# Optimization experiments

Measured on AMD Instinct MI355X. Metric: run time of the kernel, lower is better.

The kernel has to match this reference:

```python
import jax, jax.numpy as jnp
import numpy as np

# Model constants (match init_kwargs)
DIM = 256
H = 8
HD = DIM // H          # 32
WIN = 5                # spatial window_size
QS = 4                 # quant_size
CQS = 2 * QS           # color_quant_size = 8
CWIN = 2               # color_windowsize
W = 64                 # voxels per window (equal-size windows for the reference)
L_XYZ = WIN * QS       # 20 -> table length 40
L_RGB = CWIN * CQS     # 16 -> table length 32


def setup_inputs() -> dict:
    key = jax.random.key(0)
    ks = jax.random.split(key, 12)
    N = 8192
    feats = jax.random.normal(ks[0], (N, DIM), dtype=jnp.float32)
    xyz = jax.random.uniform(ks[1], (N, 3), dtype=jnp.float32) * WIN    # [0, window_size)
    rgb = jax.random.uniform(ks[2], (N, 3), dtype=jnp.float32) * CWIN   # [0, color_windowsize)
    n_coords = jnp.concatenate([xyz, rgb], axis=1)
    std = 0.02
    xyz_shape = (3, 2 * L_XYZ, H, HD)
    rgb_shape = (3, 2 * L_RGB, H, HD)
    return {
        "feats": feats,
        "n_coords": n_coords,
        "qkv_w": jax.random.normal(ks[3], (3 * DIM, DIM), dtype=jnp.float32) * std,
        "qkv_b": jnp.zeros((3 * DIM,), dtype=jnp.float32),
        "q_xyz_t": jax.random.normal(ks[4], xyz_shape, dtype=jnp.float32) * std,
        "k_xyz_t": jax.random.normal(ks[5], xyz_shape, dtype=jnp.float32) * std,
        "v_xyz_t": jax.random.normal(ks[6], xyz_shape, dtype=jnp.float32) * std,
        "q_rgb_t": jax.random.normal(ks[7], rgb_shape, dtype=jnp.float32) * std,
        "k_rgb_t": jax.random.normal(ks[8], rgb_shape, dtype=jnp.float32) * std,
        "v_rgb_t": jax.random.normal(ks[9], rgb_shape, dtype=jnp.float32) * std,
        "proj_w": jax.random.normal(ks[10], (DIM, DIM), dtype=jnp.float32) * std,
        "proj_b": jnp.zeros((DIM,), dtype=jnp.float32),
    }


def _attn_bias(q, k, idx, q_table, k_table):
    """Relative-signal bias added to QK logits.
    q,k: [nw, W, H, hd]; idx: [nw, W, W, 3] int; tables: [3, T, H, hd].
    bias[n,h,i,j] = sum_c q[n,i,h]. q_table[c, idx[n,i,j,c], h] + k[n,j,h]. k_table[c, idx, h]
    Returns (bias [nw,H,W,W], one_hot [nw,W,W,3,T]) so the one-hot is reused for the value bias.
    """
    T = q_table.shape[1]
    oh = jax.nn.one_hot(idx, T, dtype=q.dtype)                # [nw,W,W,3,T]
    dq = jnp.einsum('nihd,cthd->nicht', q, q_table)           # per-voxel dot vs all table rows
    dk = jnp.einsum('njhd,cthd->njcht', k, k_table)
    bias_q = jnp.einsum('nicht,nijct->nhij', dq, oh)
    bias_k = jnp.einsum('njcht,nijct->nhij', dk, oh)
    return bias_q + bias_k, oh


def _value_bias(attn, oh, v_table):
    """out[n,i,h,:] += sum_j attn[n,h,i,j] * sum_c v_table[c, idx[n,i,j,c], h, :]"""
    at = jnp.einsum('nhij,nijct->nhict', attn, oh)            # scatter attn mass onto table rows
    return jnp.einsum('nhict,cthd->nihd', at, v_table)


def reference(feats, n_coords, qkv_w, qkv_b, q_xyz_t, k_xyz_t, v_xyz_t,
              q_rgb_t, k_rgb_t, v_rgb_t, proj_w, proj_b):
    N = feats.shape[0]
    nw = N // W
    scale = HD ** (-0.5)

    # QKV projection, split into per-window heads
    qkv = (feats @ qkv_w.T + qkv_b).reshape(nw, W, 3, H, HD)
    q = qkv[:, :, 0] * scale
    k = qkv[:, :, 1]
    v = qkv[:, :, 2]

    # Quantized relative-signal indices (coordinate deltas, offset to [0, 2L))
    scaled = jnp.concatenate(
        [n_coords[:, 0:3] * QS, n_coords[:, 3:6] * CQS], axis=1)   # [N, 6]
    cw = scaled.reshape(nw, W, 6)
    delta = jnp.floor(cw[:, :, None, :] - cw[:, None, :, :]).astype(jnp.int32)
    offs = jnp.array([L_XYZ] * 3 + [L_RGB] * 3, dtype=jnp.int32)
    hi = jnp.array([2 * L_XYZ - 1] * 3 + [2 * L_RGB - 1] * 3, dtype=jnp.int32)
    idx = jnp.clip(delta + offs, 0, hi)                        # [nw, W, W, 6]
    idx_xyz, idx_rgb = idx[..., :3], idx[..., 3:]

    bias_x, oh_x = _attn_bias(q, k, idx_xyz, q_xyz_t, k_xyz_t)
    bias_r, oh_r = _attn_bias(q, k, idx_rgb, q_rgb_t, k_rgb_t)

    logits = jnp.einsum('nihd,njhd->nhij', q, k) + bias_x + bias_r
    attn = jax.nn.softmax(logits, axis=-1)

    out = (jnp.einsum('nhij,njhd->nihd', attn, v)
           + _value_bias(attn, oh_x, v_xyz_t)
           + _value_bias(attn, oh_r, v_rgb_t))
    out = out.reshape(N, DIM)
    return out @ proj_w.T + proj_b
```

## Files before the change

kernel.cpp:

```cpp
#include <hip/hip_runtime.h>


typedef __attribute__((ext_vector_type(8))) short short8;
typedef __attribute__((ext_vector_type(4))) float f32x4;

__device__ __forceinline__ unsigned short f2bf(float f) {
    union { float f; unsigned int u; } v; v.f = f;
    unsigned int r = v.u + 0x7FFFu + ((v.u >> 16) & 1u);
    return (unsigned short)(r >> 16);
}

#define LFENCE() asm volatile("s_waitcnt lgkmcnt(0)" ::: "memory")

__global__ __launch_bounds__(256) void k_cast(
    const float* __restrict__ feats, const float* __restrict__ qkvw,
    const float* __restrict__ pw,
    ushort* __restrict__ fb, ushort* __restrict__ qwb, ushort* __restrict__ pwb)
{
    int t = blockIdx.x * 256 + threadIdx.x;
    const float* src; ushort* dst; int off;
    if (t < 262144)            { src = feats; dst = fb;  off = t; }
    else if (t < 286720)       { src = qkvw;  dst = qwb; off = t - 262144; }
    else                       { src = pw;    dst = pwb; off = t - 286720; }
    const float* s = src + (size_t)off * 8;
    float4 v0 = *(const float4*)s, v1 = *(const float4*)(s + 4);
    union { ushort u[8]; uint4 v; } pk;
    pk.u[0] = f2bf(v0.x); pk.u[1] = f2bf(v0.y); pk.u[2] = f2bf(v0.z); pk.u[3] = f2bf(v0.w);
    pk.u[4] = f2bf(v1.x); pk.u[5] = f2bf(v1.y); pk.u[6] = f2bf(v1.z); pk.u[7] = f2bf(v1.w);
    *(uint4*)(dst + (size_t)off * 8) = pk.v;
}

__global__ __launch_bounds__(256) void k_qkv(
    const ushort* __restrict__ A, const ushort* __restrict__ B,
    const float* __restrict__ bias,
    ushort* __restrict__ qb, ushort* __restrict__ kb, ushort* __restrict__ vb)
{
    __shared__ __align__(16) ushort a_s[64 * 72];
    __shared__ __align__(16) ushort b_s[64 * 72];
    const int tid = threadIdx.x;
    const int m0 = blockIdx.y * 64;
    const int n0 = blockIdx.x * 64;
    const int w = tid >> 6, wm = w >> 1, wn = w & 1;
    const int l4 = tid & 15, quad = (tid >> 4) & 3;
    f32x4 acc[2][2];
#pragma unroll
    for (int mt = 0; mt < 2; ++mt)
#pragma unroll
        for (int nt = 0; nt < 2; ++nt) acc[mt][nt] = (f32x4){0.f, 0.f, 0.f, 0.f};

    for (int k0 = 0; k0 < 256; k0 += 64) {
#pragma unroll
        for (int l = 0; l < 2; ++l) {
            int e = tid + l * 256;
            int row = e >> 3, kq = e & 7;
            *(uint4*)&a_s[row * 72 + kq * 8] =
                *(const uint4*)(A + (size_t)(m0 + row) * 256 + k0 + kq * 8);
            *(uint4*)&b_s[row * 72 + kq * 8] =
                *(const uint4*)(B + (size_t)(n0 + row) * 256 + k0 + kq * 8);
        }
        __syncthreads();
#pragma unroll
        for (int kh = 0; kh < 2; ++kh) {
            short8 bf0 = *(const short8*)&b_s[(wn * 32 + l4) * 72 + kh * 32 + quad * 8];
            short8 bf1 = *(const short8*)&b_s[(wn * 32 + 16 + l4) * 72 + kh * 32 + quad * 8];
#pragma unroll
            for (int mt = 0; mt < 2; ++mt) {
                short8 af = *(const short8*)&a_s[(wm * 32 + mt * 16 + l4) * 72 + kh * 32 + quad * 8];
                acc[mt][0] = __builtin_amdgcn_mfma_f32_16x16x32_bf16(af, bf0, acc[mt][0], 0, 0, 0);
                acc[mt][1] = __builtin_amdgcn_mfma_f32_16x16x32_bf16(af, bf1, acc[mt][1], 0, 0, 0);
            }
        }
        __syncthreads();
    }
#pragma unroll
    for (int nt = 0; nt < 2; ++nt) {
        int c = n0 + wn * 32 + nt * 16 + l4;
        float bv = bias[c];
        int s = c >> 8, rem = c & 255, h = rem >> 5, d = rem & 31;
        ushort* dst = (s == 0) ? qb : ((s == 1) ? kb : vb);
        float mul = (s == 0) ? 0.17677669529663687f : 1.0f;
#pragma unroll
        for (int mt = 0; mt < 2; ++mt) {
            int mbase = m0 + wm * 32 + mt * 16 + quad * 4;
#pragma unroll
            for (int reg = 0; reg < 4; ++reg) {
                int m = mbase + reg;
                int nw = m >> 6, ii = m & 63;
                dst[((size_t)((nw * 8 + h) * 64 + ii)) * 32 + d] = f2bf((acc[mt][nt][reg] + bv) * mul);
            }
        }
    }
}

#define DBS 44
#define SL3 132
#define FXS 16777216.0f
#define FXI (1.0f / 16777216.0f)

__global__ __launch_bounds__(256, 2) void k_bias(
    const ushort* __restrict__ qb, const ushort* __restrict__ kb,
    const float* __restrict__ nco,
    const float* __restrict__ kxt, const float* __restrict__ krt,
    float* __restrict__ lgt)
{
    __shared__ __align__(16) float dbuf[64 * DBS];
    __shared__ __align__(16) ushort q_s[64 * 40];
    __shared__ __align__(16) ushort k_s[64 * 40];
    __shared__ __align__(16) ushort tbl[128 * 40];
    __shared__ __align__(16) float cwf[64 * 6];

    const int tid = threadIdx.x;
    const int n = blockIdx.x >> 3;
    const int h = blockIdx.x & 7;
    const int w = tid >> 6;
    const int l4 = tid & 15;
    const int quad = (tid >> 4) & 3;

    const size_t base = (size_t)((n * 8 + h) * 64) * 32;

    {
        int row = tid >> 2, part = tid & 3;
        *(uint4*)&q_s[row * 40 + part * 8] = *(const uint4*)(qb + base + tid * 8);
        *(uint4*)&k_s[row * 40 + part * 8] = *(const uint4*)(kb + base + tid * 8);
    }
    if (tid < 64) {
        const float* cp = nco + (size_t)(n * 64 + tid) * 6;
        cwf[tid * 6 + 0] = cp[0] * 4.f; cwf[tid * 6 + 1] = cp[1] * 4.f;
        cwf[tid * 6 + 2] = cp[2] * 4.f; cwf[tid * 6 + 3] = cp[3] * 8.f;
        cwf[tid * 6 + 4] = cp[4] * 8.f; cwf[tid * 6 + 5] = cp[5] * 8.f;
    }

    auto stageTbl = [&](const float* tbg, int R, int Rpad) {
        for (int e = tid; e < R * 4; e += 256) {
            int r = e >> 2, part = e & 3;
            const float* src = tbg + (size_t)r * 256 + part * 8;
            float4 f0 = *(const float4*)src, f1 = *(const float4*)(src + 4);
            union { ushort u[8]; uint4 v; } pk;
            pk.u[0] = f2bf(f0.x); pk.u[1] = f2bf(f0.y); pk.u[2] = f2bf(f0.z); pk.u[3] = f2bf(f0.w);
            pk.u[4] = f2bf(f1.x); pk.u[5] = f2bf(f1.y); pk.u[6] = f2bf(f1.z); pk.u[7] = f2bf(f1.w);
            *(uint4*)&tbl[r * 40 + part * 8] = pk.v;
        }
        for (int e = tid; e < (Rpad - R) * 40; e += 256) tbl[R * 40 + e] = 0;
    };

    float lg[4][4];
    int ibase[4];
#pragma unroll
    for (int r = 0; r < 4; ++r) ibase[r] = (w * 16 + quad * 4 + r) * DBS;

    auto tgemmC = [&](const ushort* a_s, int c, int T) {
        short8 af = *(const short8*)&a_s[(w * 16 + l4) * 40 + quad * 8];
        const int NT = (T == 40) ? 3 : 2;
        for (int tt = 0; tt < NT; ++tt) {
            short8 bf = *(const short8*)&tbl[(c * T + tt * 16 + l4) * 40 + quad * 8];
            f32x4 a = {0.f, 0.f, 0.f, 0.f};
            a = __builtin_amdgcn_mfma_f32_16x16x32_bf16(af, bf, a, 0, 0, 0);
            int col = tt * 16 + l4;
            int rb = w * 16 + quad * 4;
            if (col < T) {
                dbuf[(rb + 0) * DBS + col] = a[0];
                dbuf[(rb + 1) * DBS + col] = a[1];
                dbuf[(rb + 2) * DBS + col] = a[2];
                dbuf[(rb + 3) * DBS + col] = a[3];
            }
        }
    };

    stageTbl(kxt + h * 32, 120, 128);
    __syncthreads();

    unsigned idxp[24];
#pragma unroll
    for (int c6 = 0; c6 < 6; ++c6) {
        const int off = (c6 < 3) ? 20 : 16, hi = (c6 < 3) ? 39 : 31;
        float co0 = cwf[(w * 16 + quad * 4 + 0) * 6 + c6];
        float co1 = cwf[(w * 16 + quad * 4 + 1) * 6 + c6];
        float co2 = cwf[(w * 16 + quad * 4 + 2) * 6 + c6];
        float co3 = cwf[(w * 16 + quad * 4 + 3) * 6 + c6];
#pragma unroll
        for (int tt = 0; tt < 4; ++tt) {
            float ci = cwf[(tt * 16 + l4) * 6 + c6];
            unsigned p = (unsigned)min(max((int)floorf(ci - co0) + off, 0), hi);
            p |= (unsigned)min(max((int)floorf(ci - co1) + off, 0), hi) << 8;
            p |= (unsigned)min(max((int)floorf(ci - co2) + off, 0), hi) << 16;
            p |= (unsigned)min(max((int)floorf(ci - co3) + off, 0), hi) << 24;
            idxp[c6 * 4 + tt] = p;
        }
    }

    auto gatherT = [&](int cc) {
#pragma unroll
        for (int tt = 0; tt < 4; ++tt) {
            unsigned p = idxp[cc * 4 + tt];
#pragma unroll
            for (int r = 0; r < 4; ++r) {
                int x = (p >> (8 * r)) & 255;
                lg[tt][r] += dbuf[ibase[r] + x];
            }
        }
    };

    {
        short8 ak = *(const short8*)&k_s[(w * 16 + l4) * 40 + quad * 8];
#pragma unroll
        for (int tt = 0; tt < 4; ++tt) {
            short8 bq = *(const short8*)&q_s[(tt * 16 + l4) * 40 + quad * 8];
            f32x4 r = {0.f, 0.f, 0.f, 0.f};
            r = __builtin_amdgcn_mfma_f32_16x16x32_bf16(ak, bq, r, 0, 0, 0);
            lg[tt][0] = r[0]; lg[tt][1] = r[1]; lg[tt][2] = r[2]; lg[tt][3] = r[3];
        }
    }

    tgemmC(k_s, 0, 40); LFENCE();
    gatherT(0); LFENCE();
    tgemmC(k_s, 1, 40); LFENCE();
    gatherT(1); LFENCE();
    tgemmC(k_s, 2, 40); LFENCE();
    gatherT(2);
    __syncthreads();
    stageTbl(krt + h * 32, 96, 96);
    __syncthreads();
    tgemmC(k_s, 0, 32); LFENCE();
    gatherT(3); LFENCE();
    tgemmC(k_s, 1, 32); LFENCE();
    gatherT(4); LFENCE();
    tgemmC(k_s, 2, 32); LFENCE();
    gatherT(5);

    {
        float* lp = lgt + (size_t)(n * 8 + h) * 4096;
#pragma unroll
        for (int tt = 0; tt < 4; ++tt)
#pragma unroll
            for (int reg = 0; reg < 4; ++reg)
                lp[(w * 16 + quad * 4 + reg) * 64 + tt * 16 + l4] = lg[tt][reg];
    }
}

__global__ __launch_bounds__(256, 2) void k_av(
    const ushort* __restrict__ qb, const ushort* __restrict__ vb,
    const float* __restrict__ nco,
    const float* __restrict__ qxt, const float* __restrict__ vxt,
    const float* __restrict__ qrt, const float* __restrict__ vrt,
    const float* __restrict__ lgt,
    ushort* __restrict__ aout)
{
    __shared__ __align__(16) float dbuf[64 * SL3];
    __shared__ __align__(16) ushort U[11264];
    __shared__ __align__(16) float cwf[64 * 6];
    ushort* q_s  = U;
    ushort* tbl  = U + 2560;
    ushort* attn_s = U;
    ushort* v_t    = U + 4608;
    ushort* vtbl   = U + 6912;

    const int tid = threadIdx.x;
    const int n = blockIdx.x >> 3;
    const int h = blockIdx.x & 7;
    const int w = tid >> 6;
    const int lane = tid & 63;
    const int l4 = tid & 15;
    const int quad = (tid >> 4) & 3;

    const size_t base = (size_t)((n * 8 + h) * 64) * 32;

    {
        int row = tid >> 2, part = tid & 3;
        *(uint4*)&q_s[row * 40 + part * 8] = *(const uint4*)(qb + base + tid * 8);
    }
    if (tid < 64) {
        const float* cp = nco + (size_t)(n * 64 + tid) * 6;
        cwf[tid * 6 + 0] = cp[0] * 4.f; cwf[tid * 6 + 1] = cp[1] * 4.f;
        cwf[tid * 6 + 2] = cp[2] * 4.f; cwf[tid * 6 + 3] = cp[3] * 8.f;
        cwf[tid * 6 + 4] = cp[4] * 8.f; cwf[tid * 6 + 5] = cp[5] * 8.f;
    }

    auto stageTbl = [&](const float* tbg, int R, int Rpad) {
        for (int e = tid; e < R * 4; e += 256) {
            int r = e >> 2, part = e & 3;
            const float* src = tbg + (size_t)r * 256 + part * 8;
            float4 f0 = *(const float4*)src, f1 = *(const float4*)(src + 4);
            union { ushort u[8]; uint4 v; } pk;
            pk.u[0] = f2bf(f0.x); pk.u[1] = f2bf(f0.y); pk.u[2] = f2bf(f0.z); pk.u[3] = f2bf(f0.w);
            pk.u[4] = f2bf(f1.x); pk.u[5] = f2bf(f1.y); pk.u[6] = f2bf(f1.z); pk.u[7] = f2bf(f1.w);
            *(uint4*)&tbl[r * 40 + part * 8] = pk.v;
        }
        for (int e = tid; e < (Rpad - R) * 40; e += 256) tbl[R * 40 + e] = 0;
    };
    auto stageVtbl = [&](const float* tbg, int R) {
        for (int e = tid; e < R * 4; e += 256) {
            int r = e >> 2, part = e & 3;
            const float* src = tbg + (size_t)r * 256 + part * 8;
            float4 f0 = *(const float4*)src, f1 = *(const float4*)(src + 4);
            int d0 = part * 8;
            vtbl[(d0 + 0) * 136 + r] = f2bf(f0.x);
            vtbl[(d0 + 1) * 136 + r] = f2bf(f0.y);
            vtbl[(d0 + 2) * 136 + r] = f2bf(f0.z);
            vtbl[(d0 + 3) * 136 + r] = f2bf(f0.w);
            vtbl[(d0 + 4) * 136 + r] = f2bf(f1.x);
            vtbl[(d0 + 5) * 136 + r] = f2bf(f1.y);
            vtbl[(d0 + 6) * 136 + r] = f2bf(f1.z);
            vtbl[(d0 + 7) * 136 + r] = f2bf(f1.w);
        }
    };
    auto stageVt = [&]() {
        int j = tid >> 2, d0 = (tid & 3) * 8;
        uint4 pk = *(const uint4*)(vb + base + tid * 8);
        const ushort* u = (const ushort*)&pk;
#pragma unroll
        for (int ii = 0; ii < 8; ++ii) v_t[(d0 + ii) * 72 + j] = u[ii];
    };

    float lg[4][4];
    {
        const float* lp = lgt + (size_t)(n * 8 + h) * 4096;
        int i0 = w * 16 + quad * 4;
#pragma unroll
        for (int tt = 0; tt < 4; ++tt) {
            f32x4 v = *(const f32x4*)(lp + (size_t)(tt * 16 + l4) * 64 + i0);
            lg[tt][0] = v[0]; lg[tt][1] = v[1]; lg[tt][2] = v[2]; lg[tt][3] = v[3];
        }
    }

    int ibase[4];
#pragma unroll
    for (int r = 0; r < 4; ++r) ibase[r] = (w * 16 + quad * 4 + r) * SL3;

    auto tgemm3 = [&](int T) {
        short8 af = *(const short8*)&q_s[(w * 16 + l4) * 40 + quad * 8];
        const int NT = (T == 40) ? 3 : 2;
        int rb = w * 16 + quad * 4;
#pragma unroll
        for (int c = 0; c < 3; ++c) {
            for (int tt = 0; tt < NT; ++tt) {
                short8 bf = *(const short8*)&tbl[(c * T + tt * 16 + l4) * 40 + quad * 8];
                f32x4 a = {0.f, 0.f, 0.f, 0.f};
                a = __builtin_amdgcn_mfma_f32_16x16x32_bf16(af, bf, a, 0, 0, 0);
                int col = tt * 16 + l4;
                if (col < T) {
                    int sc = c * DBS + col;
                    dbuf[(rb + 0) * SL3 + sc] = a[0];
                    dbuf[(rb + 1) * SL3 + sc] = a[1];
                    dbuf[(rb + 2) * SL3 + sc] = a[2];
                    dbuf[(rb + 3) * SL3 + sc] = a[3];
                }
            }
        }
    };
    auto zeroAll = [&]() {
        float4 z = {0.f, 0.f, 0.f, 0.f};
        float4* rb = (float4*)&dbuf[w * 16 * SL3];
        for (int v = lane; v < 528; v += 64) rb[v] = z;
    };

    stageTbl(qxt + h * 32, 120, 128);
    __syncthreads();

    unsigned idxp[24];
#pragma unroll
    for (int c6 = 0; c6 < 6; ++c6) {
        const int off = (c6 < 3) ? 20 : 16, hi = (c6 < 3) ? 39 : 31;
        float co0 = cwf[(w * 16 + quad * 4 + 0) * 6 + c6];
        float co1 = cwf[(w * 16 + quad * 4 + 1) * 6 + c6];
        float co2 = cwf[(w * 16 + quad * 4 + 2) * 6 + c6];
        float co3 = cwf[(w * 16 + quad * 4 + 3) * 6 + c6];
#pragma unroll
        for (int tt = 0; tt < 4; ++tt) {
            float cj = cwf[(tt * 16 + l4) * 6 + c6];
            unsigned p = (unsigned)min(max((int)floorf(co0 - cj) + off, 0), hi);
            p |= (unsigned)min(max((int)floorf(co1 - cj) + off, 0), hi) << 8;
            p |= (unsigned)min(max((int)floorf(co2 - cj) + off, 0), hi) << 16;
            p |= (unsigned)min(max((int)floorf(co3 - cj) + off, 0), hi) << 24;
            idxp[c6 * 4 + tt] = p;
        }
    }

    auto gather3 = [&](int half) {
#pragma unroll
        for (int c = 0; c < 3; ++c) {
#pragma unroll
            for (int tt = 0; tt < 4; ++tt) {
                unsigned p = idxp[(half * 3 + c) * 4 + tt];
#pragma unroll
                for (int r = 0; r < 4; ++r) {
                    int x = (p >> (8 * r)) & 255;
                    lg[tt][r] += dbuf[ibase[r] + c * DBS + x];
                }
            }
        }
    };
    auto scatter3 = [&](int half) {
        unsigned* bb = (unsigned*)dbuf;
#pragma unroll
        for (int c = 0; c < 3; ++c) {
#pragma unroll
            for (int tt = 0; tt < 4; ++tt) {
                unsigned p = idxp[(half * 3 + c) * 4 + tt];
#pragma unroll
                for (int r = 0; r < 4; ++r) {
                    int x = (p >> (8 * r)) & 255;
                    unsigned q = (unsigned)(lg[tt][r] * FXS + 0.5f);
                    atomicAdd(&bb[ibase[r] + c * DBS + x], q);
                }
            }
        }
    };

    tgemm3(40);
    __syncthreads();
    gather3(0);
    stageTbl(qrt + h * 32, 96, 96);
    __syncthreads();
    tgemm3(32);
    __syncthreads();
    gather3(1);
    stageVtbl(vxt + h * 32, 120);
    stageVt();
    __syncthreads();

#pragma unroll
    for (int reg = 0; reg < 4; ++reg) {
        float m = fmaxf(fmaxf(lg[0][reg], lg[1][reg]), fmaxf(lg[2][reg], lg[3][reg]));
        m = fmaxf(m, __shfl_xor(m, 1));
        m = fmaxf(m, __shfl_xor(m, 2));
        m = fmaxf(m, __shfl_xor(m, 4));
        m = fmaxf(m, __shfl_xor(m, 8));
        float s = 0.f;
#pragma unroll
        for (int tt = 0; tt < 4; ++tt) { lg[tt][reg] = __expf(lg[tt][reg] - m); s += lg[tt][reg]; }
        s += __shfl_xor(s, 1); s += __shfl_xor(s, 2);
        s += __shfl_xor(s, 4); s += __shfl_xor(s, 8);
        float inv = 1.f / s;
#pragma unroll
        for (int tt = 0; tt < 4; ++tt) lg[tt][reg] *= inv;
    }
#pragma unroll
    for (int tt = 0; tt < 4; ++tt)
#pragma unroll
        for (int reg = 0; reg < 4; ++reg)
            attn_s[(w * 16 + quad * 4 + reg) * 72 + tt * 16 + l4] = f2bf(lg[tt][reg]);
    zeroAll();
    __syncthreads();

    f32x4 acc0 = {0.f, 0.f, 0.f, 0.f}, acc1 = {0.f, 0.f, 0.f, 0.f};
#pragma unroll
    for (int s = 0; s < 2; ++s) {
        short8 af = *(const short8*)&attn_s[(w * 16 + l4) * 72 + s * 32 + quad * 8];
        short8 b0 = *(const short8*)&v_t[l4 * 72 + s * 32 + quad * 8];
        short8 b1 = *(const short8*)&v_t[(16 + l4) * 72 + s * 32 + quad * 8];
        acc0 = __builtin_amdgcn_mfma_f32_16x16x32_bf16(af, b0, acc0, 0, 0, 0);
        acc1 = __builtin_amdgcn_mfma_f32_16x16x32_bf16(af, b1, acc1, 0, 0, 0);
    }

    auto atgemm3 = [&](int T, int S) {
        int rowb = (w * 16 + l4) * SL3;
#pragma unroll
        for (int c = 0; c < 3; ++c) {
#pragma unroll
            for (int s = 0; s < S; ++s) {
                int koff = s * 32 + quad * 8;
                short8 af = {0, 0, 0, 0, 0, 0, 0, 0};
                int kr = 0;
                if (koff < T) {
                    const unsigned* ap = (const unsigned*)&dbuf[rowb + c * DBS + koff];
                    uint4 u0 = *(const uint4*)ap;
                    uint4 u1 = *(const uint4*)(ap + 4);
                    af[0] = (short)f2bf((float)u0.x * FXI); af[1] = (short)f2bf((float)u0.y * FXI);
                    af[2] = (short)f2bf((float)u0.z * FXI); af[3] = (short)f2bf((float)u0.w * FXI);
                    af[4] = (short)f2bf((float)u1.x * FXI); af[5] = (short)f2bf((float)u1.y * FXI);
                    af[6] = (short)f2bf((float)u1.z * FXI); af[7] = (short)f2bf((float)u1.w * FXI);
                    kr = c * T + koff;
                }
                short8 b0 = *(const short8*)&vtbl[l4 * 136 + kr];
                short8 b1 = *(const short8*)&vtbl[(16 + l4) * 136 + kr];
                acc0 = __builtin_amdgcn_mfma_f32_16x16x32_bf16(af, b0, acc0, 0, 0, 0);
                acc1 = __builtin_amdgcn_mfma_f32_16x16x32_bf16(af, b1, acc1, 0, 0, 0);
            }
        }
    };

    scatter3(0); LFENCE();
    atgemm3(40, 2);
    __syncthreads();
    zeroAll();
    stageVtbl(vrt + h * 32, 96);
    __syncthreads();
    scatter3(1); LFENCE();
    atgemm3(32, 1);

    {
        ushort* op = aout + (size_t)(n * 64 + w * 16 + quad * 4) * 256 + h * 32;
#pragma unroll
        for (int reg = 0; reg < 4; ++reg) {
            op[reg * 256 + l4] = f2bf(acc0[reg]);
            op[reg * 256 + 16 + l4] = f2bf(acc1[reg]);
        }
    }
}

__global__ __launch_bounds__(256) void k_proj(
    const ushort* __restrict__ A, const ushort* __restrict__ B,
    const float* __restrict__ bias, float* __restrict__ out)
{
    __shared__ __align__(16) ushort a_s[64 * 72];
    __shared__ __align__(16) ushort b_s[64 * 72];
    const int tid = threadIdx.x;
    const int m0 = blockIdx.y * 64;
    const int n0 = blockIdx.x * 64;
    const int w = tid >> 6, wm = w >> 1, wn = w & 1;
    const int l4 = tid & 15, quad = (tid >> 4) & 3;
    f32x4 acc[2][2];
#pragma unroll
    for (int mt = 0; mt < 2; ++mt)
#pragma unroll
        for (int nt = 0; nt < 2; ++nt) acc[mt][nt] = (f32x4){0.f, 0.f, 0.f, 0.f};

    for (int k0 = 0; k0 < 256; k0 += 64) {
#pragma unroll
        for (int l = 0; l < 2; ++l) {
            int e = tid + l * 256;
            int row = e >> 3, kq = e & 7;
            *(uint4*)&a_s[row * 72 + kq * 8] =
                *(const uint4*)(A + (size_t)(m0 + row) * 256 + k0 + kq * 8);
            *(uint4*)&b_s[row * 72 + kq * 8] =
                *(const uint4*)(B + (size_t)(n0 + row) * 256 + k0 + kq * 8);
        }
        __syncthreads();
#pragma unroll
        for (int kh = 0; kh < 2; ++kh) {
            short8 bf0 = *(const short8*)&b_s[(wn * 32 + l4) * 72 + kh * 32 + quad * 8];
            short8 bf1 = *(const short8*)&b_s[(wn * 32 + 16 + l4) * 72 + kh * 32 + quad * 8];
#pragma unroll
            for (int mt = 0; mt < 2; ++mt) {
                short8 af = *(const short8*)&a_s[(wm * 32 + mt * 16 + l4) * 72 + kh * 32 + quad * 8];
                acc[mt][0] = __builtin_amdgcn_mfma_f32_16x16x32_bf16(af, bf0, acc[mt][0], 0, 0, 0);
                acc[mt][1] = __builtin_amdgcn_mfma_f32_16x16x32_bf16(af, bf1, acc[mt][1], 0, 0, 0);
            }
        }
        __syncthreads();
    }
#pragma unroll
    for (int nt = 0; nt < 2; ++nt) {
        int c = n0 + wn * 32 + nt * 16 + l4;
        float bv = bias[c];
#pragma unroll
        for (int mt = 0; mt < 2; ++mt) {
            int mbase = m0 + wm * 32 + mt * 16 + quad * 4;
#pragma unroll
            for (int reg = 0; reg < 4; ++reg)
                out[(size_t)(mbase + reg) * 256 + c] = acc[mt][nt][reg] + bv;
        }
    }
}

extern "C" void kernel_launch(void* const* d_in, const int* in_sizes, int n_in,
                              void* d_out, int out_size, void* d_ws, size_t ws_size,
                              hipStream_t stream)
{
    const float* feats = (const float*)d_in[0];
    const float* nco   = (const float*)d_in[1];
    const float* qkvw  = (const float*)d_in[2];
    const float* qkvb  = (const float*)d_in[3];
    const float* qxt   = (const float*)d_in[4];
    const float* kxt   = (const float*)d_in[5];
    const float* vxt   = (const float*)d_in[6];
    const float* qrt   = (const float*)d_in[7];
    const float* krt   = (const float*)d_in[8];
    const float* vrt   = (const float*)d_in[9];
    const float* pw    = (const float*)d_in[10];
    const float* pb    = (const float*)d_in[11];
    float* out = (float*)d_out;

    ushort* qb  = (ushort*)d_ws;
    ushort* kb  = qb + (size_t)2097152;
    ushort* vb  = kb + (size_t)2097152;
    ushort* aob = vb + (size_t)2097152;
    float*  lgt = (float*)(aob + (size_t)2097152);
    ushort* fb  = (ushort*)(lgt + (size_t)4194304);
    ushort* qwb = fb + (size_t)2097152;
    ushort* pwb = qwb + (size_t)196608;

    k_cast<<<dim3(1152), 256, 0, stream>>>(feats, qkvw, pw, fb, qwb, pwb);
    k_qkv<<<dim3(12, 128), 256, 0, stream>>>(fb, qwb, qkvb, qb, kb, vb);
    k_bias<<<dim3(1024), 256, 0, stream>>>(qb, kb, nco, kxt, krt, lgt);
    k_av<<<dim3(1024), 256, 0, stream>>>(qb, vb, nco, qxt, vxt, qrt, vrt, lgt, aob);
    k_proj<<<dim3(4, 128), 256, 0, stream>>>(aob, pwb, pb, out);
}
```

Baseline: 148.4 us.

## Fuse key-bias logits kernel into attention kernel, dropping logits round-trip

Merges the separate key-side bias kernel into the attention/value kernel, so QK logits and both key and query table biases are computed in registers within one block. This removes a 16 MB fp32 logits write and read through global memory and one kernel launch. In exchange the fused kernel does more serial work per block, with extra table staging and syncthreads, and it must fit K in the same shared buffer, which may lengthen each block.

```diff
diff --git a/kernel.cpp b/kernel.cpp
--- a/kernel.cpp
+++ b/kernel.cpp
@@ -97,159 +97,19 @@
 #define FXS 16777216.0f
 #define FXI (1.0f / 16777216.0f)
 
-__global__ __launch_bounds__(256, 2) void k_bias(
-    const ushort* __restrict__ qb, const ushort* __restrict__ kb,
+__global__ __launch_bounds__(256, 2) void k_attn(
+    const ushort* __restrict__ qb, const ushort* __restrict__ kb, const ushort* __restrict__ vb,
     const float* __restrict__ nco,
-    const float* __restrict__ kxt, const float* __restrict__ krt,
-    float* __restrict__ lgt)
-{
-    __shared__ __align__(16) float dbuf[64 * DBS];
-    __shared__ __align__(16) ushort q_s[64 * 40];
-    __shared__ __align__(16) ushort k_s[64 * 40];
-    __shared__ __align__(16) ushort tbl[128 * 40];
-    __shared__ __align__(16) float cwf[64 * 6];
-
-    const int tid = threadIdx.x;
-    const int n = blockIdx.x >> 3;
-    const int h = blockIdx.x & 7;
-    const int w = tid >> 6;
-    const int l4 = tid & 15;
-    const int quad = (tid >> 4) & 3;
-
-    const size_t base = (size_t)((n * 8 + h) * 64) * 32;
-
-    {
-        int row = tid >> 2, part = tid & 3;
-        *(uint4*)&q_s[row * 40 + part * 8] = *(const uint4*)(qb + base + tid * 8);
-        *(uint4*)&k_s[row * 40 + part * 8] = *(const uint4*)(kb + base + tid * 8);
-    }
-    if (tid < 64) {
-        const float* cp = nco + (size_t)(n * 64 + tid) * 6;
-        cwf[tid * 6 + 0] = cp[0] * 4.f; cwf[tid * 6 + 1] = cp[1] * 4.f;
-        cwf[tid * 6 + 2] = cp[2] * 4.f; cwf[tid * 6 + 3] = cp[3] * 8.f;
-        cwf[tid * 6 + 4] = cp[4] * 8.f; cwf[tid * 6 + 5] = cp[5] * 8.f;
-    }
-
-    auto stageTbl = [&](const float* tbg, int R, int Rpad) {
-        for (int e = tid; e < R * 4; e += 256) {
-            int r = e >> 2, part = e & 3;
-            const float* src = tbg + (size_t)r * 256 + part * 8;
-            float4 f0 = *(const float4*)src, f1 = *(const float4*)(src + 4);
-            union { ushort u[8]; uint4 v; } pk;
-            pk.u[0] = f2bf(f0.x); pk.u[1] = f2bf(f0.y); pk.u[2] = f2bf(f0.z); pk.u[3] = f2bf(f0.w);
-            pk.u[4] = f2bf(f1.x); pk.u[5] = f2bf(f1.y); pk.u[6] = f2bf(f1.z); pk.u[7] = f2bf(f1.w);
-            *(uint4*)&tbl[r * 40 + part * 8] = pk.v;
-        }
-        for (int e = tid; e < (Rpad - R) * 40; e += 256) tbl[R * 40 + e] = 0;
-    };
-
-    float lg[4][4];
-    int ibase[4];
-#pragma unroll
-    for (int r = 0; r < 4; ++r) ibase[r] = (w * 16 + quad * 4 + r) * DBS;
-
-    auto tgemmC = [&](const ushort* a_s, int c, int T) {
-        short8 af = *(const short8*)&a_s[(w * 16 + l4) * 40 + quad * 8];
-        const int NT = (T == 40) ? 3 : 2;
-        for (int tt = 0; tt < NT; ++tt) {
-            short8 bf = *(const short8*)&tbl[(c * T + tt * 16 + l4) * 40 + quad * 8];
-            f32x4 a = {0.f, 0.f, 0.f, 0.f};
-            a = __builtin_amdgcn_mfma_f32_16x16x32_bf16(af, bf, a, 0, 0, 0);
-            int col = tt * 16 + l4;
-            int rb = w * 16 + quad * 4;
-            if (col < T) {
-                dbuf[(rb + 0) * DBS + col] = a[0];
-                dbuf[(rb + 1) * DBS + col] = a[1];
-                dbuf[(rb + 2) * DBS + col] = a[2];
-                dbuf[(rb + 3) * DBS + col] = a[3];
-            }
-        }
-    };
-
-    stageTbl(kxt + h * 32, 120, 128);
-    __syncthreads();
-
-    unsigned idxp[24];
-#pragma unroll
-    for (int c6 = 0; c6 < 6; ++c6) {
-        const int off = (c6 < 3) ? 20 : 16, hi = (c6 < 3) ? 39 : 31;
-        float co0 = cwf[(w * 16 + quad * 4 + 0) * 6 + c6];
-        float co1 = cwf[(w * 16 + quad * 4 + 1) * 6 + c6];
-        float co2 = cwf[(w * 16 + quad * 4 + 2) * 6 + c6];
-        float co3 = cwf[(w * 16 + quad * 4 + 3) * 6 + c6];
-#pragma unroll
-        for (int tt = 0; tt < 4; ++tt) {
-            float ci = cwf[(tt * 16 + l4) * 6 + c6];
-            unsigned p = (unsigned)min(max((int)floorf(ci - co0) + off, 0), hi);
-            p |= (unsigned)min(max((int)floorf(ci - co1) + off, 0), hi) << 8;
-            p |= (unsigned)min(max((int)floorf(ci - co2) + off, 0), hi) << 16;
-            p |= (unsigned)min(max((int)floorf(ci - co3) + off, 0), hi) << 24;
-            idxp[c6 * 4 + tt] = p;
-        }
-    }
-
-    auto gatherT = [&](int cc) {
-#pragma unroll
-        for (int tt = 0; tt < 4; ++tt) {
-            unsigned p = idxp[cc * 4 + tt];
-#pragma unroll
-            for (int r = 0; r < 4; ++r) {
-                int x = (p >> (8 * r)) & 255;
-                lg[tt][r] += dbuf[ibase[r] + x];
-            }
-        }
-    };
-
-    {
-        short8 ak = *(const short8*)&k_s[(w * 16 + l4) * 40 + quad * 8];
-#pragma unroll
-        for (int tt = 0; tt < 4; ++tt) {
-            short8 bq = *(const short8*)&q_s[(tt * 16 + l4) * 40 + quad * 8];
-            f32x4 r = {0.f, 0.f, 0.f, 0.f};
-            r = __builtin_amdgcn_mfma_f32_16x16x32_bf16(ak, bq, r, 0, 0, 0);
-            lg[tt][0] = r[0]; lg[tt][1] = r[1]; lg[tt][2] = r[2]; lg[tt][3] = r[3];
-        }
-    }
-
-    tgemmC(k_s, 0, 40); LFENCE();
-    gatherT(0); LFENCE();
-    tgemmC(k_s, 1, 40); LFENCE();
-    gatherT(1); LFENCE();
-    tgemmC(k_s, 2, 40); LFENCE();
-    gatherT(2);
-    __syncthreads();
-    stageTbl(krt + h * 32, 96, 96);
-    __syncthreads();
-    tgemmC(k_s, 0, 32); LFENCE();
-    gatherT(3); LFENCE();
-    tgemmC(k_s, 1, 32); LFENCE();
-    gatherT(4); LFENCE();
-    tgemmC(k_s, 2, 32); LFENCE();
-    gatherT(5);
-
-    {
-        float* lp = lgt + (size_t)(n * 8 + h) * 4096;
-#pragma unroll
-        for (int tt = 0; tt < 4; ++tt)
-#pragma unroll
-            for (int reg = 0; reg < 4; ++reg)
-                lp[(w * 16 + quad * 4 + reg) * 64 + tt * 16 + l4] = lg[tt][reg];
-    }
-}
-
-__global__ __launch_bounds__(256, 2) void k_av(
-    const ushort* __restrict__ qb, const ushort* __restrict__ vb,
-    const float* __restrict__ nco,
-    const float* __restrict__ qxt, const float* __restrict__ vxt,
-    const float* __restrict__ qrt, const float* __restrict__ vrt,
-    const float* __restrict__ lgt,
+    const float* __restrict__ qxt, const float* __restrict__ kxt, const float* __restrict__ vxt,
+    const float* __restrict__ qrt, const float* __restrict__ krt, const float* __restrict__ vrt,
     ushort* __restrict__ aout)
 {
     __shared__ __align__(16) float dbuf[64 * SL3];
     __shared__ __align__(16) ushort U[11264];
     __shared__ __align__(16) float cwf[64 * 6];
     ushort* q_s  = U;
-    ushort* tbl  = U + 2560;
+    ushort* k_s  = U + 2560;
+    ushort* tbl  = U + 5120;
     ushort* attn_s = U;
     ushort* v_t    = U + 4608;
     ushort* vtbl   = U + 6912;
@@ -267,6 +127,7 @@
     {
         int row = tid >> 2, part = tid & 3;
         *(uint4*)&q_s[row * 40 + part * 8] = *(const uint4*)(qb + base + tid * 8);
+        *(uint4*)&k_s[row * 40 + part * 8] = *(const uint4*)(kb + base + tid * 8);
     }
     if (tid < 64) {
         const float* cp = nco + (size_t)(n * 64 + tid) * 6;
@@ -311,14 +172,38 @@
         for (int ii = 0; ii < 8; ++ii) v_t[(d0 + ii) * 72 + j] = u[ii];
     };
 
+    stageTbl(kxt + h * 32, 120, 128);
+    __syncthreads();
+
+    unsigned idxp[24];
+#pragma unroll
+    for (int c6 = 0; c6 < 6; ++c6) {
+        const int off = (c6 < 3) ? 20 : 16, hi = (c6 < 3) ? 39 : 31;
+        float co0 = cwf[(w * 16 + quad * 4 + 0) * 6 + c6];
+        float co1 = cwf[(w * 16 + quad * 4 + 1) * 6 + c6];
+        float co2 = cwf[(w * 16 + quad * 4 + 2) * 6 + c6];
+        float co3 = cwf[(w * 16 + quad * 4 + 3) * 6 + c6];
+#pragma unroll
+        for (int tt = 0; tt < 4; ++tt) {
+            float cj = cwf[(tt * 16 + l4) * 6 + c6];
+            unsigned p = (unsigned)min(max((int)floorf(co0 - cj) + off, 0), hi);
+            p |= (unsigned)min(max((int)floorf(co1 - cj) + off, 0), hi) << 8;
+            p |= (unsigned)min(max((int)floorf(co2 - cj) + off, 0), hi) << 16;
+            p |= (unsigned)min(max((int)floorf(co3 - cj) + off, 0), hi) << 24;
+            idxp[c6 * 4 + tt] = p;
+        }
+    }
+
     float lg[4][4];
+
     {
-        const float* lp = lgt + (size_t)(n * 8 + h) * 4096;
-        int i0 = w * 16 + quad * 4;
+        short8 aq = *(const short8*)&q_s[(w * 16 + l4) * 40 + quad * 8];
 #pragma unroll
         for (int tt = 0; tt < 4; ++tt) {
-            f32x4 v = *(const f32x4*)(lp + (size_t)(tt * 16 + l4) * 64 + i0);
-            lg[tt][0] = v[0]; lg[tt][1] = v[1]; lg[tt][2] = v[2]; lg[tt][3] = v[3];
+            short8 bk = *(const short8*)&k_s[(tt * 16 + l4) * 40 + quad * 8];
+            f32x4 r = {0.f, 0.f, 0.f, 0.f};
+            r = __builtin_amdgcn_mfma_f32_16x16x32_bf16(aq, bk, r, 0, 0, 0);
+            lg[tt][0] = r[0]; lg[tt][1] = r[1]; lg[tt][2] = r[2]; lg[tt][3] = r[3];
         }
     }
 
@@ -326,8 +211,8 @@
 #pragma unroll
     for (int r = 0; r < 4; ++r) ibase[r] = (w * 16 + quad * 4 + r) * SL3;
 
-    auto tgemm3 = [&](int T) {
-        short8 af = *(const short8*)&q_s[(w * 16 + l4) * 40 + quad * 8];
+    auto tgemm3 = [&](const ushort* a_sp, int T) {
+        short8 af = *(const short8*)&a_sp[(w * 16 + l4) * 40 + quad * 8];
         const int NT = (T == 40) ? 3 : 2;
         int rb = w * 16 + quad * 4;
 #pragma unroll
@@ -347,35 +232,22 @@
             }
         }
     };
-    auto zeroAll = [&]() {
-        float4 z = {0.f, 0.f, 0.f, 0.f};
-        float4* rb = (float4*)&dbuf[w * 16 * SL3];
-        for (int v = lane; v < 528; v += 64) rb[v] = z;
-    };
-
-    stageTbl(qxt + h * 32, 120, 128);
-    __syncthreads();
-
-    unsigned idxp[24];
-#pragma unroll
-    for (int c6 = 0; c6 < 6; ++c6) {
-        const int off = (c6 < 3) ? 20 : 16, hi = (c6 < 3) ? 39 : 31;
-        float co0 = cwf[(w * 16 + quad * 4 + 0) * 6 + c6];
-        float co1 = cwf[(w * 16 + quad * 4 + 1) * 6 + c6];
-        float co2 = cwf[(w * 16 + quad * 4 + 2) * 6 + c6];
-        float co3 = cwf[(w * 16 + quad * 4 + 3) * 6 + c6];
-#pragma unroll
-        for (int tt = 0; tt < 4; ++tt) {
-            float cj = cwf[(tt * 16 + l4) * 6 + c6];
-            unsigned p = (unsigned)min(max((int)floorf(co0 - cj) + off, 0), hi);
-            p |= (unsigned)min(max((int)floorf(co1 - cj) + off, 0), hi) << 8;
-            p |= (unsigned)min(max((int)floorf(co2 - cj) + off, 0), hi) << 16;
-            p |= (unsigned)min(max((int)floorf(co3 - cj) + off, 0), hi) << 24;
-            idxp[c6 * 4 + tt] = p;
-        }
-    }
-
-    auto gather3 = [&](int half) {
+    auto gatherK3 = [&](int half) {
+#pragma unroll
+        for (int c = 0; c < 3; ++c) {
+#pragma unroll
+            for (int tt = 0; tt < 4; ++tt) {
+                unsigned p = idxp[(half * 3 + c) * 4 + tt];
+                int jb = (tt * 16 + l4) * SL3 + c * DBS;
+#pragma unroll
+                for (int r = 0; r < 4; ++r) {
+                    int x = (p >> (8 * r)) & 255;
+                    lg[tt][r] += dbuf[jb + x];
+                }
+            }
+        }
+    };
+    auto gatherQ3 = [&](int half) {
 #pragma unroll
         for (int c = 0; c < 3; ++c) {
 #pragma unroll
@@ -405,15 +277,32 @@
             }
         }
     };
-
-    tgemm3(40);
-    __syncthreads();
-    gather3(0);
+    auto zeroAll = [&]() {
+        float4 z = {0.f, 0.f, 0.f, 0.f};
+        float4* rb = (float4*)&dbuf[w * 16 * SL3];
+        for (int v = lane; v < 528; v += 64) rb[v] = z;
+    };
+
+    tgemm3(k_s, 40);
+    __syncthreads();
+    gatherK3(0);
+    __syncthreads();
+    stageTbl(krt + h * 32, 96, 96);
+    __syncthreads();
+    tgemm3(k_s, 32);
+    __syncthreads();
+    gatherK3(1);
+    __syncthreads();
+    stageTbl(qxt + h * 32, 120, 128);
+    __syncthreads();
+    tgemm3(q_s, 40);
+    __syncthreads();
+    gatherQ3(0);
     stageTbl(qrt + h * 32, 96, 96);
     __syncthreads();
-    tgemm3(32);
-    __syncthreads();
-    gather3(1);
+    tgemm3(q_s, 32);
+    __syncthreads();
+    gatherQ3(1);
     stageVtbl(vxt + h * 32, 120);
     stageVt();
     __syncthreads();
@@ -575,14 +464,12 @@
     ushort* kb  = qb + (size_t)2097152;
     ushort* vb  = kb + (size_t)2097152;
     ushort* aob = vb + (size_t)2097152;
-    float*  lgt = (float*)(aob + (size_t)2097152);
-    ushort* fb  = (ushort*)(lgt + (size_t)4194304);
+    ushort* fb  = aob + (size_t)2097152;
     ushort* qwb = fb + (size_t)2097152;
     ushort* pwb = qwb + (size_t)196608;
 
     k_cast<<<dim3(1152), 256, 0, stream>>>(feats, qkvw, pw, fb, qwb, pwb);
     k_qkv<<<dim3(12, 128), 256, 0, stream>>>(fb, qwb, qkvb, qb, kb, vb);
-    k_bias<<<dim3(1024), 256, 0, stream>>>(qb, kb, nco, kxt, krt, lgt);
-    k_av<<<dim3(1024), 256, 0, stream>>>(qb, vb, nco, qxt, vxt, qrt, vrt, lgt, aob);
+    k_attn<<<dim3(1024), 256, 0, stream>>>(qb, kb, vb, nco, qxt, kxt, vxt, qrt, krt, vrt, aob);
     k_proj<<<dim3(4, 128), 256, 0, stream>>>(aob, pwb, pb, out);
 }
```

New measurement: 188.8 us. +27.3%, slower.
